# Kernel tuning notes

Hardware: AMD Instinct MI355X
Metric: run time of the kernel (lower is better)

Reference implementation:

```python
import jax, jax.numpy as jnp
import numpy as np

NEG_INF = -1e9  # large negative for masked softmax (bf16-safe)
LEAKY_SLOPE = 0.2


def setup_inputs() -> dict:
    key = jax.random.key(0)
    k1, k2, k3, k4, k5 = jax.random.split(key, 5)
    N, F_in, F_out = 8192, 128, 128
    X = jax.random.normal(k1, (N, F_in), dtype=jnp.float32)
    A = jax.random.randint(k2, (N, N), 0, 2, dtype=jnp.int32)  # dense 0/1 adjacency
    W = jax.random.normal(k3, (F_in, F_out), dtype=jnp.float32) * (F_in ** -0.5)
    a_src = jax.random.normal(k4, (F_out,), dtype=jnp.float32) * (F_out ** -0.5)
    a_dst = jax.random.normal(k5, (F_out,), dtype=jnp.float32) * (F_out ** -0.5)
    return {"X": X, "A": A, "W": W, "a_src": a_src, "a_dst": a_dst}


def reference(X, A, W, a_src, a_dst):
    # Linear projection: [N, F_out]
    H = X @ W
    # Additive attention logits: e_ij = LeakyReLU(a_src . h_i + a_dst . h_j)
    es = H @ a_src  # [N] contribution of destination/center node i
    ed = H @ a_dst  # [N] contribution of source/neighbor node j
    e = es[:, None] + ed[None, :]                      # [N, N]
    e = jnp.where(e > 0, e, LEAKY_SLOPE * e)           # LeakyReLU(0.2)
    # Mask to adjacency with self-loops, softmax over neighbors j
    mask = (A > 0) | jnp.eye(A.shape[0], dtype=bool)
    e = jnp.where(mask, e, NEG_INF)
    alpha = jax.nn.softmax(e, axis=1)                  # [N, N]
    # Weighted aggregation + ELU nonlinearity
    out = alpha @ H                                    # [N, F_out]
    return jax.nn.elu(out)
```

## Files before the change

kernel.cpp:

```cpp
#include <hip/hip_runtime.h>
#include <hip/hip_bf16.h>


typedef __bf16 bf16_t;
typedef bf16_t bf16x8 __attribute__((ext_vector_type(8)));
typedef float  f32x4  __attribute__((ext_vector_type(4)));
typedef int    i32x4  __attribute__((ext_vector_type(4)));

#define NN 8192
#define DD 128
#define JSPLIT 4

__global__ __launch_bounds__(512) void k1_fused(const float* __restrict__ X,
                                                const float* __restrict__ W,
                                                const float* __restrict__ a_src,
                                                const float* __restrict__ a_dst,
                                                float* __restrict__ es,
                                                float* __restrict__ edv,
                                                bf16_t* __restrict__ VB) {
  __shared__ float Wl[DD * DD];
  __shared__ bf16_t Tl[DD][40];
  const int t = threadIdx.x;
  const int rb = blockIdx.x << 5;

  if (t < 256) {
    const int k = t & 127;
    const float* av = (t < 128) ? a_src : a_dst;
    const f32x4* wrow = (const f32x4*)(W + k * DD);
    float s = 0.f;
    #pragma unroll
    for (int c4 = 0; c4 < 32; ++c4) {
      const f32x4 wv = wrow[c4];
      const f32x4 avv = *(const f32x4*)(av + c4 * 4);
      s += wv[0] * avv[0] + wv[1] * avv[1] + wv[2] * avv[2] + wv[3] * avv[3];
    }
    Wl[t] = s;
  }
  if (t < 64) Wl[256 + t] = 0.f;
  __syncthreads();

  {
    const int r = t >> 4, part = t & 15;
    const f32x4* xrow = (const f32x4*)(X + (size_t)(rb + r) * DD + part * 8);
    float s = 0.f, d = 0.f;
    #pragma unroll
    for (int q = 0; q < 2; ++q) {
      const f32x4 xv = xrow[q];
      const f32x4 sv = *(const f32x4*)(Wl + part * 8 + q * 4);
      const f32x4 dv = *(const f32x4*)(Wl + 128 + part * 8 + q * 4);
      s += xv[0] * sv[0] + xv[1] * sv[1] + xv[2] * sv[2] + xv[3] * sv[3];
      d += xv[0] * dv[0] + xv[1] * dv[1] + xv[2] * dv[2] + xv[3] * dv[3];
    }
    atomicAdd(&Wl[256 + r], s);
    atomicAdd(&Wl[288 + r], d);
  }
  __syncthreads();
  if (t < 32) {
    es[rb + t] = Wl[256 + t];
  } else if (t < 64) {
    edv[rb + t - 32] = Wl[288 + t - 32];
  }
  __syncthreads();

  for (int idx = t; idx < DD * DD; idx += 512) Wl[idx] = W[idx];
  __syncthreads();

  const int c = t & 127;
  const int r0 = t >> 7;
  for (int rr = 0; rr < 8; ++rr) {
    const int r = (rr << 2) + r0;
    const f32x4* xrow = (const f32x4*)(X + (size_t)(rb + r) * DD);
    float acc = 0.f;
    #pragma unroll
    for (int k4 = 0; k4 < 32; ++k4) {
      const f32x4 xv = xrow[k4];
      acc += xv[0] * Wl[(k4 * 4 + 0) * DD + c] + xv[1] * Wl[(k4 * 4 + 1) * DD + c] +
             xv[2] * Wl[(k4 * 4 + 2) * DD + c] + xv[3] * Wl[(k4 * 4 + 3) * DD + c];
    }
    Tl[c][r] = (bf16_t)acc;
  }
  __syncthreads();

  {
    const int cb = t >> 6;
    const int lane = t & 63;
    const int col = (cb << 4) + (lane & 15);
    const int rloc = (lane >> 4) << 3;
    const bf16x8 u = *(const bf16x8*)&Tl[col][rloc];
    *(bf16x8*)(VB + ((((size_t)(rb >> 5) << 3) + cb) * 64 + lane) * 8) = u;
  }
}

__global__ __launch_bounds__(256, 3) void k2_gat(const int* __restrict__ A,
                                                 const float* __restrict__ es,
                                                 const float* __restrict__ edv,
                                                 const bf16_t* __restrict__ VB,
                                                 float* __restrict__ num,
                                                 float* __restrict__ denP) {
  __shared__ float ML[16 * DD];
  __shared__ float denL[16];
  const int t = threadIdx.x;
  const int lane = t & 63, ws = t >> 6;
  const int l16 = lane & 15, lk = lane >> 4;
  const int rb = (blockIdx.x >> 2) << 4;
  const int jq = blockIdx.x & 3;
  const int jq0 = jq << 11;
  const int jbase = jq0 + (ws << 9);

  const int r0 = rb + l16;
  const float es0 = es[r0];

  const int* pA = A + (size_t)r0 * NN + jbase + (lk << 3);
  const float* ped = edv + jbase + (lk << 3);
  const bf16_t* pV = VB + (((size_t)(jbase >> 5) << 3) * 64 + lane) * 8;
  const int jth0 = jbase + (lk << 3);

  f32x4 acc[8];
  #pragma unroll
  for (int cb = 0; cb < 8; ++cb) acc[cb] = f32x4{0.f, 0.f, 0.f, 0.f};
  float dsum = 0.f;

  i32x4 aA0 = *(const i32x4*)pA, aB0 = *(const i32x4*)(pA + 4);
  f32x4 eA0 = *(const f32x4*)ped, eB0 = *(const f32x4*)(ped + 4);
  i32x4 aA1 = *(const i32x4*)(pA + 32), aB1 = *(const i32x4*)(pA + 36);
  f32x4 eA1 = *(const f32x4*)(ped + 32), eB1 = *(const f32x4*)(ped + 36);

  auto step = [&](int it, i32x4& aA, i32x4& aB, f32x4& eA, f32x4& eB) {
    const bf16_t* pvi = pV + (size_t)it * 4096;
    bf16x8 vb[8];
    #pragma unroll
    for (int cb = 0; cb < 8; ++cb) vb[cb] = *(const bf16x8*)(pvi + (cb << 9));
    const int jit = jth0 + (it << 5);
    bf16x8 pa;
    float s = 0.f;
    #pragma unroll
    for (int e = 0; e < 8; ++e) {
      const int av = (e < 4) ? aA[e] : aB[e - 4];
      const float edq = (e < 4) ? eA[e] : eB[e - 4];
      float x = es0 + edq;
      x = fmaxf(x, 0.2f * x);
      const float p = (av > 0 || (jit + e) == r0) ? __expf(x) : 0.f;
      s += p;
      pa[e] = (bf16_t)p;
    }
    dsum += s;
    if (it + 2 < 16) {
      const int off = (it + 2) << 5;
      aA = *(const i32x4*)(pA + off);
      aB = *(const i32x4*)(pA + off + 4);
      eA = *(const f32x4*)(ped + off);
      eB = *(const f32x4*)(ped + off + 4);
    }
    #pragma unroll
    for (int cb = 0; cb < 8; ++cb)
      acc[cb] = __builtin_amdgcn_mfma_f32_16x16x32_bf16(pa, vb[cb], acc[cb], 0, 0, 0);
  };

  #pragma unroll 1
  for (int it2 = 0; it2 < 8; ++it2) {
    step(2 * it2, aA0, aB0, eA0, eB0);
    step(2 * it2 + 1, aA1, aB1, eA1, eB1);
  }

  dsum += __shfl_xor(dsum, 16, 64);
  dsum += __shfl_xor(dsum, 32, 64);
  if (t < 16) denL[t] = 0.f;
  for (int i = t; i < 16 * DD; i += 256) ML[i] = 0.f;
  __syncthreads();
  if (lane < 16) atomicAdd(&denL[lane], dsum);
  #pragma unroll
  for (int cb = 0; cb < 8; ++cb) {
    #pragma unroll
    for (int rg = 0; rg < 4; ++rg) {
      atomicAdd(&ML[((lk << 2) + rg) * DD + (cb << 4) + l16], acc[cb][rg]);
    }
  }
  __syncthreads();
  {
    const int row = t >> 4;
    const int c0 = (t & 15) << 3;
    float* nq = num + (size_t)jq * (NN * DD) + (size_t)(rb + row) * DD + c0;
    *(f32x4*)nq = *(const f32x4*)&ML[row * DD + c0];
    *(f32x4*)(nq + 4) = *(const f32x4*)&ML[row * DD + c0 + 4];
  }
  if (t < 16) denP[(size_t)jq * NN + rb + t] = denL[t];
}

__global__ __launch_bounds__(256) void k3_fin(const float* __restrict__ num,
                                              const float* __restrict__ denP,
                                              float* __restrict__ out) {
  const int g = blockIdx.x * 256 + threadIdx.x;
  const size_t b = (size_t)g * 8;
  const int row = (int)(b >> 7);
  float den = 0.f;
  #pragma unroll
  for (int q = 0; q < JSPLIT; ++q) den += denP[(size_t)q * NN + row];
  const float rd = 1.f / den;
  f32x4 s0 = {0.f, 0.f, 0.f, 0.f}, s1 = {0.f, 0.f, 0.f, 0.f};
  #pragma unroll
  for (int q = 0; q < JSPLIT; ++q) {
    const float* nb = num + (size_t)q * (NN * DD);
    s0 += *(const f32x4*)(nb + b);
    s1 += *(const f32x4*)(nb + b + 4);
  }
  #pragma unroll
  for (int e = 0; e < 4; ++e) {
    float v = s0[e] * rd;
    s0[e] = v > 0.f ? v : (__expf(v) - 1.f);
    v = s1[e] * rd;
    s1[e] = v > 0.f ? v : (__expf(v) - 1.f);
  }
  *(f32x4*)(out + b) = s0;
  *(f32x4*)(out + b + 4) = s1;
}

extern "C" void kernel_launch(void* const* d_in, const int* in_sizes, int n_in,
                              void* d_out, int out_size, void* d_ws, size_t ws_size,
                              hipStream_t stream) {
  const float* X = (const float*)d_in[0];
  const int* A = (const int*)d_in[1];
  const float* W = (const float*)d_in[2];
  const float* a_src = (const float*)d_in[3];
  const float* a_dst = (const float*)d_in[4];
  float* out = (float*)d_out;

  char* w = (char*)d_ws;
  bf16_t* VB = (bf16_t*)(w + 0);
  float* es = (float*)(w + 2097152);
  float* edv = (float*)(w + 2129920);
  float* denP = (float*)(w + 2162688);
  float* num = (float*)(w + 2293760);

  hipLaunchKernelGGL(k1_fused, dim3(256), dim3(512), 0, stream, X, W, a_src, a_dst, es,
                     edv, VB);
  hipLaunchKernelGGL(k2_gat, dim3(2048), dim3(256), 0, stream, A, es, edv, VB, num,
                     denP);
  hipLaunchKernelGGL(k3_fin, dim3(512), dim3(256), 0, stream, num, denP, out);
}
```

Baseline: 156.2 us.

## Pack adjacency into bitmask in a pre-pass and retile the attention kernel

Adds a kernel that reads the dense int32 adjacency once, packs it into 32-bit bitmasks with the self-loop diagonal folded in, and passes those to the attention kernel. The attention kernel is retiled so each 512-thread block covers 64 rows, with waves split by row group and column half, and it prefetches V fragments two steps ahead. The shared-memory atomic reduction is removed and each wave writes its partial results to global memory directly. The pre-pass still has to stream the full 256MB adjacency, so this mainly saves the strided reads and per-element work inside the MFMA loop, while adding one extra launch and an 8MB intermediate buffer.

```diff
diff --git a/kernel.cpp b/kernel.cpp
--- a/kernel.cpp
+++ b/kernel.cpp
@@ -10,6 +10,25 @@
 #define NN 8192
 #define DD 128
 #define JSPLIT 4
+
+__global__ __launch_bounds__(256) void kA_pack(const int* __restrict__ A,
+                                               unsigned* __restrict__ bits) {
+  const int w = blockIdx.x * 256 + threadIdx.x;
+  const i32x4* p = (const i32x4*)(A + (size_t)w * 32);
+  i32x4 v[8];
+  #pragma unroll
+  for (int q = 0; q < 8; ++q) v[q] = p[q];
+  unsigned m = 0;
+  #pragma unroll
+  for (int q = 0; q < 8; ++q) {
+    #pragma unroll
+    for (int e = 0; e < 4; ++e) m |= ((unsigned)v[q][e]) << (q * 4 + e);
+  }
+  const int row = w >> 8;
+  const int c0 = (w & 255) << 5;
+  if (row >= c0 && row < c0 + 32) m |= 1u << (row - c0);
+  bits[w] = m;
+}
 
 __global__ __launch_bounds__(512) void k1_fused(const float* __restrict__ X,
                                                 const float* __restrict__ W,
@@ -91,99 +110,102 @@
   }
 }
 
-__global__ __launch_bounds__(256, 3) void k2_gat(const int* __restrict__ A,
+__global__ __launch_bounds__(512, 4) void k2_gat(const unsigned* __restrict__ bits,
                                                  const float* __restrict__ es,
                                                  const float* __restrict__ edv,
                                                  const bf16_t* __restrict__ VB,
                                                  float* __restrict__ num,
                                                  float* __restrict__ denP) {
-  __shared__ float ML[16 * DD];
-  __shared__ float denL[16];
   const int t = threadIdx.x;
-  const int lane = t & 63, ws = t >> 6;
+  const int lane = t & 63, wave = t >> 6;
   const int l16 = lane & 15, lk = lane >> 4;
-  const int rb = (blockIdx.x >> 2) << 4;
+  const int rg = wave >> 1, ch = wave & 1;
+  const int rb = (blockIdx.x >> 2) << 6;
   const int jq = blockIdx.x & 3;
   const int jq0 = jq << 11;
-  const int jbase = jq0 + (ws << 9);
-
-  const int r0 = rb + l16;
+
+  const int r0 = rb + (rg << 4) + l16;
   const float es0 = es[r0];
 
-  const int* pA = A + (size_t)r0 * NN + jbase + (lk << 3);
-  const float* ped = edv + jbase + (lk << 3);
-  const bf16_t* pV = VB + (((size_t)(jbase >> 5) << 3) * 64 + lane) * 8;
-  const int jth0 = jbase + (lk << 3);
-
-  f32x4 acc[8];
-  #pragma unroll
-  for (int cb = 0; cb < 8; ++cb) acc[cb] = f32x4{0.f, 0.f, 0.f, 0.f};
+  const unsigned* pB = bits + (size_t)r0 * 256 + (jq << 6);
+  const float* ped = edv + jq0 + (lk << 3);
+  const bf16_t* pV = VB + ((((size_t)(jq << 6)) * 8 + (ch << 2)) * 64 + lane) * 8;
+
+  f32x4 acc[4];
+  #pragma unroll
+  for (int cf = 0; cf < 4; ++cf) acc[cf] = f32x4{0.f, 0.f, 0.f, 0.f};
   float dsum = 0.f;
 
-  i32x4 aA0 = *(const i32x4*)pA, aB0 = *(const i32x4*)(pA + 4);
-  f32x4 eA0 = *(const f32x4*)ped, eB0 = *(const f32x4*)(ped + 4);
-  i32x4 aA1 = *(const i32x4*)(pA + 32), aB1 = *(const i32x4*)(pA + 36);
-  f32x4 eA1 = *(const f32x4*)(ped + 32), eB1 = *(const f32x4*)(ped + 36);
-
-  auto step = [&](int it, i32x4& aA, i32x4& aB, f32x4& eA, f32x4& eB) {
-    const bf16_t* pvi = pV + (size_t)it * 4096;
-    bf16x8 vb[8];
-    #pragma unroll
-    for (int cb = 0; cb < 8; ++cb) vb[cb] = *(const bf16x8*)(pvi + (cb << 9));
-    const int jit = jth0 + (it << 5);
+  unsigned bw0, bw1;
+  f32x4 eA0, eB0, eA1, eB1;
+  bf16x8 v00, v01, v02, v03, v10, v11, v12, v13;
+
+  bw0 = pB[0];
+  bw1 = pB[1];
+  eA0 = *(const f32x4*)ped;
+  eB0 = *(const f32x4*)(ped + 4);
+  eA1 = *(const f32x4*)(ped + 32);
+  eB1 = *(const f32x4*)(ped + 36);
+  v00 = *(const bf16x8*)(pV);
+  v01 = *(const bf16x8*)(pV + 512);
+  v02 = *(const bf16x8*)(pV + 1024);
+  v03 = *(const bf16x8*)(pV + 1536);
+  v10 = *(const bf16x8*)(pV + 4096);
+  v11 = *(const bf16x8*)(pV + 4096 + 512);
+  v12 = *(const bf16x8*)(pV + 4096 + 1024);
+  v13 = *(const bf16x8*)(pV + 4096 + 1536);
+
+  auto step = [&](int s, unsigned& bw, f32x4& eA, f32x4& eB, bf16x8& w0, bf16x8& w1,
+                  bf16x8& w2, bf16x8& w3) {
+    const unsigned mb = bw >> (lk << 3);
     bf16x8 pa;
-    float s = 0.f;
+    float ps = 0.f;
     #pragma unroll
     for (int e = 0; e < 8; ++e) {
-      const int av = (e < 4) ? aA[e] : aB[e - 4];
       const float edq = (e < 4) ? eA[e] : eB[e - 4];
       float x = es0 + edq;
       x = fmaxf(x, 0.2f * x);
-      const float p = (av > 0 || (jit + e) == r0) ? __expf(x) : 0.f;
-      s += p;
+      const float p = ((mb >> e) & 1u) ? __expf(x) : 0.f;
+      ps += p;
       pa[e] = (bf16_t)p;
     }
-    dsum += s;
-    if (it + 2 < 16) {
-      const int off = (it + 2) << 5;
-      aA = *(const i32x4*)(pA + off);
-      aB = *(const i32x4*)(pA + off + 4);
-      eA = *(const f32x4*)(ped + off);
-      eB = *(const f32x4*)(ped + off + 4);
-    }
-    #pragma unroll
-    for (int cb = 0; cb < 8; ++cb)
-      acc[cb] = __builtin_amdgcn_mfma_f32_16x16x32_bf16(pa, vb[cb], acc[cb], 0, 0, 0);
+    dsum += ps;
+    acc[0] = __builtin_amdgcn_mfma_f32_16x16x32_bf16(pa, w0, acc[0], 0, 0, 0);
+    acc[1] = __builtin_amdgcn_mfma_f32_16x16x32_bf16(pa, w1, acc[1], 0, 0, 0);
+    acc[2] = __builtin_amdgcn_mfma_f32_16x16x32_bf16(pa, w2, acc[2], 0, 0, 0);
+    acc[3] = __builtin_amdgcn_mfma_f32_16x16x32_bf16(pa, w3, acc[3], 0, 0, 0);
+    if (s + 2 < 64) {
+      const int o = (s + 2) << 5;
+      bw = pB[s + 2];
+      eA = *(const f32x4*)(ped + o);
+      eB = *(const f32x4*)(ped + o + 4);
+      const bf16_t* pv = pV + (size_t)(s + 2) * 4096;
+      w0 = *(const bf16x8*)(pv);
+      w1 = *(const bf16x8*)(pv + 512);
+      w2 = *(const bf16x8*)(pv + 1024);
+      w3 = *(const bf16x8*)(pv + 1536);
+    }
   };
 
   #pragma unroll 1
-  for (int it2 = 0; it2 < 8; ++it2) {
-    step(2 * it2, aA0, aB0, eA0, eB0);
-    step(2 * it2 + 1, aA1, aB1, eA1, eB1);
+  for (int g = 0; g < 32; ++g) {
+    step(2 * g, bw0, eA0, eB0, v00, v01, v02, v03);
+    step(2 * g + 1, bw1, eA1, eB1, v10, v11, v12, v13);
   }
 
   dsum += __shfl_xor(dsum, 16, 64);
   dsum += __shfl_xor(dsum, 32, 64);
-  if (t < 16) denL[t] = 0.f;
-  for (int i = t; i < 16 * DD; i += 256) ML[i] = 0.f;
-  __syncthreads();
-  if (lane < 16) atomicAdd(&denL[lane], dsum);
-  #pragma unroll
-  for (int cb = 0; cb < 8; ++cb) {
-    #pragma unroll
-    for (int rg = 0; rg < 4; ++rg) {
-      atomicAdd(&ML[((lk << 2) + rg) * DD + (cb << 4) + l16], acc[cb][rg]);
-    }
-  }
-  __syncthreads();
-  {
-    const int row = t >> 4;
-    const int c0 = (t & 15) << 3;
-    float* nq = num + (size_t)jq * (NN * DD) + (size_t)(rb + row) * DD + c0;
-    *(f32x4*)nq = *(const f32x4*)&ML[row * DD + c0];
-    *(f32x4*)(nq + 4) = *(const f32x4*)&ML[row * DD + c0 + 4];
-  }
-  if (t < 16) denP[(size_t)jq * NN + rb + t] = denL[t];
+  if (ch == 0 && lane < 16) denP[(size_t)jq * NN + r0] = dsum;
+
+  float* nq = num + (size_t)jq * (NN * DD);
+  #pragma unroll
+  for (int cf = 0; cf < 4; ++cf) {
+    const int col = (ch << 6) + (cf << 4) + l16;
+    #pragma unroll
+    for (int r = 0; r < 4; ++r) {
+      nq[(size_t)(rb + (rg << 4) + (lk << 2) + r) * DD + col] = acc[cf][r];
+    }
+  }
 }
 
 __global__ __launch_bounds__(256) void k3_fin(const float* __restrict__ num,
@@ -225,15 +247,17 @@
   float* out = (float*)d_out;
 
   char* w = (char*)d_ws;
-  bf16_t* VB = (bf16_t*)(w + 0);
-  float* es = (float*)(w + 2097152);
-  float* edv = (float*)(w + 2129920);
-  float* denP = (float*)(w + 2162688);
-  float* num = (float*)(w + 2293760);
-
+  unsigned* bitsv = (unsigned*)(w + 0);
+  bf16_t* VB = (bf16_t*)(w + 8388608);
+  float* es = (float*)(w + 10485760);
+  float* edv = (float*)(w + 10518528);
+  float* denP = (float*)(w + 10551296);
+  float* num = (float*)(w + 10682368);
+
+  hipLaunchKernelGGL(kA_pack, dim3(NN * NN / 32 / 256), dim3(256), 0, stream, A, bitsv);
   hipLaunchKernelGGL(k1_fused, dim3(256), dim3(512), 0, stream, X, W, a_src, a_dst, es,
                      edv, VB);
-  hipLaunchKernelGGL(k2_gat, dim3(2048), dim3(256), 0, stream, A, es, edv, VB, num,
+  hipLaunchKernelGGL(k2_gat, dim3(512), dim3(512), 0, stream, bitsv, es, edv, VB, num,
                      denP);
   hipLaunchKernelGGL(k3_fin, dim3(512), dim3(256), 0, stream, num, denP, out);
 }
```

Result: no change. 156.9 us (+0.4%).
